# Performance work log

Measured on AMD Instinct MI355X. Metric: run time of the kernel, lower is better.

## Reference

```python
import jax, jax.numpy as jnp
import numpy as np

B, L, D, CH, H = 16384, 50, 20, 16, 6


def setup_inputs() -> dict:
    key = jax.random.key(0)
    ks = jax.random.split(key, 18)
    s = 0.1
    return {
        "x": jax.random.normal(ks[0], (B, L, D), jnp.float32),
        "we_w": jax.random.normal(ks[1], (CH, D), jnp.float32) * s,
        "we_b": jax.random.normal(ks[2], (CH,), jnp.float32) * s,
        "attn_w": jax.random.normal(ks[3], (CH, CH), jnp.float32) * s,
        "attn_b": jax.random.normal(ks[4], (CH,), jnp.float32) * s,
        "conv1_w": jax.random.normal(ks[5], (CH, CH, 1), jnp.float32) * s,
        "conv1_b": jax.random.normal(ks[6], (CH,), jnp.float32) * s,
        "conv2_w": jax.random.normal(ks[7], (CH, CH, 3), jnp.float32) * s,
        "conv2_b": jax.random.normal(ks[8], (CH,), jnp.float32) * s,
        "conv3_w": jax.random.normal(ks[9], (CH, CH, 5), jnp.float32) * s,
        "conv3_b": jax.random.normal(ks[10], (CH,), jnp.float32) * s,
        "gru_wih": jax.random.normal(ks[11], (3 * H, CH), jnp.float32) * s,
        "gru_whh": jax.random.normal(ks[12], (3 * H, H), jnp.float32) * s,
        "gru_bih": jax.random.normal(ks[13], (3 * H,), jnp.float32) * s,
        "gru_bhh": jax.random.normal(ks[14], (3 * H,), jnp.float32) * s,
        "fc3_w": jax.random.normal(ks[15], (2, 3 * CH + H), jnp.float32) * s,
        "fc3_b": jax.random.normal(ks[16], (2,), jnp.float32) * s,
        "batchsize": B,
    }


def _conv1d(x, w, b, pad):
    # x: [B, C, L], w: [O, I, K] -> [B, O, L]
    y = jax.lax.conv_general_dilated(x, w, (1,), [(pad, pad)],
                                     dimension_numbers=("NCH", "OIH", "NCH"))
    return y + b[None, :, None]


def _gru(xg, wih, whh, bih, bhh):
    # xg: [B, L, CH] -> outputs [B, L, H] (PyTorch GRU equations, h0=0)
    gi = jnp.einsum("blc,gc->blg", xg, wih) + bih  # [B, L, 3H]
    gi_t = jnp.swapaxes(gi, 0, 1)                  # [L, B, 3H]
    h0 = jnp.zeros((xg.shape[0], H), xg.dtype)

    def step(h, gi_step):
        gh = h @ whh.T + bhh
        i_r, i_z, i_n = jnp.split(gi_step, 3, axis=-1)
        h_r, h_z, h_n = jnp.split(gh, 3, axis=-1)
        r = jax.nn.sigmoid(i_r + h_r)
        z = jax.nn.sigmoid(i_z + h_z)
        n = jnp.tanh(i_n + r * h_n)
        h_new = (1.0 - z) * n + z * h
        return h_new, h_new

    _, outs = jax.lax.scan(step, h0, gi_t)
    return jnp.swapaxes(outs, 0, 1)  # [B, L, H]


def reference(x, we_w, we_b, attn_w, attn_b, conv1_w, conv1_b, conv2_w, conv2_b,
              conv3_w, conv3_b, gru_wih, gru_whh, gru_bih, gru_bhh, fc3_w, fc3_b,
              batchsize):
    b = batchsize
    xe = x @ we_w.T + we_b                 # [B, L, CH]
    xr = xe.reshape(b, CH, L)              # RESHAPE (not transpose), as in torch

    lrelu = lambda v: jnp.where(v > 0, v, 0.1 * v)
    x1 = lrelu(_conv1d(xr, conv1_w, conv1_b, 0))
    x2 = lrelu(_conv1d(xr, conv2_w, conv2_b, 1))
    x3 = lrelu(_conv1d(xr, conv3_w, conv3_b, 2))

    xg = xr.reshape(b, L, CH)              # == xe
    x4 = _gru(xg, gru_wih, gru_whh, gru_bih, gru_bhh)  # [B, L, H]

    # dotproduct1: note x4.reshape([B,H,L]) is a reshape, NOT a transpose
    scores = jnp.matmul(x4, x4.reshape(b, H, L)) / H   # [B, L, L]
    alphas = jax.nn.softmax(scores, axis=1)            # softmax over dim=1 as in torch
    y = jnp.matmul(alphas, x4).reshape(b, H, L)        # [B, H, L]
    x_gru = jnp.sum(y, axis=2)                         # [B, H]

    # vectorized per-timestep attention loop: x[:, :, i] over i -> swapaxes
    xt = jnp.swapaxes(xr, 1, 2)                        # [B, L, CH]
    attn = jnp.tanh(xt @ attn_w.T + attn_b)            # [B, L, CH]
    attn1 = jnp.concatenate([attn, attn, attn], axis=2).reshape(b, 3 * CH, L)

    x_cat = jnp.concatenate([x1, x2, x3], axis=1)      # [B, 3CH, L]
    x_cnn = jnp.sum(x_cat * attn1, axis=2)             # [B, 3CH]

    feat = jnp.concatenate([x_cnn, x_gru], axis=1)     # [B, 3CH+H]
    return feat @ fc3_w.T + fc3_b                      # [B, 2]
```

## Files before the change

### kernel.cpp

```cpp
#include <hip/hip_runtime.h>

#define BATCH 16384
#define LSEQ  50
#define DIN   20
#define CHN   16
#define HID   6

typedef float vf2 __attribute__((ext_vector_type(2)));

__device__ __forceinline__ float frcp(float x){ return __builtin_amdgcn_rcpf(x); }
__device__ __forceinline__ float fsig(float x){ return frcp(1.0f + __expf(-x)); }
__device__ __forceinline__ float ftanh(float x){ float t = __expf(2.0f*x); return (t - 1.0f) * frcp(t + 1.0f); }
__device__ __forceinline__ float lrelu(float v){ return v > 0.0f ? v : 0.1f*v; }
__device__ __forceinline__ vf2 fma2(vf2 a, vf2 b, vf2 c){
#if __has_builtin(__builtin_elementwise_fma)
  return __builtin_elementwise_fma(a, b, c);
#else
  vf2 r; r.x = fmaf(a.x, b.x, c.x); r.y = fmaf(a.y, b.y, c.y); return r;
#endif
}

constexpr int SLAB = 2544;

__global__ __launch_bounds__(256, 4) void fused_kernel(
    const float* __restrict__ x,
    const float* __restrict__ we_w, const float* __restrict__ we_b,
    const float* __restrict__ attn_w, const float* __restrict__ attn_b,
    const float* __restrict__ c1w, const float* __restrict__ c1b,
    const float* __restrict__ c2w, const float* __restrict__ c2b,
    const float* __restrict__ c3w, const float* __restrict__ c3b,
    const float* __restrict__ wih, const float* __restrict__ whh,
    const float* __restrict__ bih, const float* __restrict__ bhh,
    const float* __restrict__ fc3w, const float* __restrict__ fc3b,
    float* __restrict__ out)
{
  __shared__ __align__(16) float smem[4 * SLAB];
  const int tid  = threadIdx.x;
  const int wave = tid >> 6;
  const int lane = tid & 63;
  const int b    = blockIdx.x * 4 + wave;

  float* S    = smem + wave * SLAB;
  float* sXEp = S;
  float* sY   = S;
  float* R1   = S + 840;
  float* sFE  = S + 1640;
  float* sX4  = S + 1840;
  float* sX4P = S + 2144;

  const float* xb = x + (size_t)b * (LSEQ * DIN);

  if (lane < CHN) {
    sXEp[lane * 52]     = 0.0f;
    sXEp[lane * 52 + 1] = 0.0f;
  } else if (lane == 16) {
    sXEp[832] = 0.0f;
    sXEp[833] = 0.0f;
  }

  if (lane < LSEQ) {
    vf2 xv2[10];
    const float4* xr = (const float4*)(xb + lane * DIN);
    #pragma unroll
    for (int q = 0; q < 5; ++q) {
      float4 v = xr[q];
      vf2 p0; p0.x = v.x; p0.y = v.y;
      vf2 p1; p1.x = v.z; p1.y = v.w;
      xv2[2*q] = p0; xv2[2*q+1] = p1;
    }
    float xe[CHN];
    #pragma unroll
    for (int c = 0; c < CHN; ++c) {
      const vf2* wr = (const vf2*)(we_w + c * DIN);
      vf2 a2; a2.x = we_b[c]; a2.y = 0.0f;
      #pragma unroll
      for (int dp = 0; dp < 10; ++dp) a2 = fma2(xv2[dp], wr[dp], a2);
      xe[c] = a2.x + a2.y;
    }
    const int kk0 = lane * CHN;
    const int i0  = kk0 / 50;
    const int m0  = kk0 - i0 * 50;
    float* basep = sXEp + i0 * 52 + 2 + m0;
    #pragma unroll
    for (int c = 0; c < CHN; ++c) {
      const int off = c + ((m0 + c >= 50) ? 2 : 0);
      basep[off] = xe[c];
    }
    vf2 xe2[8];
    #pragma unroll
    for (int p = 0; p < 8; ++p) { xe2[p].x = xe[2*p]; xe2[p].y = xe[2*p+1]; }
    float gi[18];
    #pragma unroll
    for (int g = 0; g < 18; ++g) {
      const vf2* wr = (const vf2*)(wih + g * CHN);
      vf2 a2; a2.x = bih[g]; a2.y = 0.0f;
      #pragma unroll
      for (int p = 0; p < 8; ++p) a2 = fma2(xe2[p], wr[p], a2);
      gi[g] = a2.x + a2.y;
    }
    float4* gd = (float4*)(R1 + lane * 20);
    gd[0] = make_float4(gi[0], gi[1], gi[2], gi[3]);
    gd[1] = make_float4(gi[4], gi[5], gi[6], gi[7]);
    gd[2] = make_float4(gi[8], gi[9], gi[10], gi[11]);
    gd[3] = make_float4(gi[12], gi[13], gi[14], gi[15]);
    *(float2*)(R1 + lane * 20 + 16) = make_float2(gi[16], gi[17]);
  }
  __syncthreads();

  if (wave == 0) {
    const int q = lane >> 4;
    const int g = lane & 15;
    const int gb = 16 + (g & 1);
    float wa[HID], wb[HID];
    #pragma unroll
    for (int k = 0; k < HID; ++k) { wa[k] = whh[g * HID + k]; wb[k] = whh[gb * HID + k]; }
    const float ba = bhh[g];
    const float bb = bhh[gb];

    float* giq  = smem + q * SLAB + 840;
    float* x4q  = smem + q * SLAB + 1840;
    float* x4pq = smem + q * SLAB + 2144;

    const int base = q << 4;
    const int srcZ = base + 6 + g;
    const int srcN = base + ((g < 4) ? (12 + g) : (g - 4));

    float hh[HID];
    #pragma unroll
    for (int k = 0; k < HID; ++k) hh[k] = 0.0f;

    for (int l = 0; l < LSEQ; ++l) {
      const float gia = giq[l * 20 + g];
      const float gib = giq[l * 20 + gb];
      float gha = ba, ghb = bb;
      #pragma unroll
      for (int k = 0; k < HID; ++k) {
        gha = fmaf(wa[k], hh[k], gha);
        ghb = fmaf(wb[k], hh[k], ghb);
      }
      const float siga = fsig(gia + gha);
      const float ghx = (g >= 12) ? gha : ghb;
      const float gix = (g >= 12) ? gia : gib;
      const float ghn = __shfl(ghx, srcN);
      const float gin = __shfl(gix, srcN);
      const float z   = __shfl(siga, srcZ);
      const float n   = ftanh(fmaf(siga, ghn, gin));
      const float hn  = fmaf(z, hh[g < HID ? g : 0] - n, n);
      if (g < HID) {
        x4q[l * HID + g] = hn;
        x4pq[l * 8 + g]  = hn;
      }
      #pragma unroll
      for (int k = 0; k < HID; ++k) hh[k] = __shfl(hn, base + k);
    }
  }
  __syncthreads();

  if (lane < LSEQ) {
    float a[CHN];
    #pragma unroll
    for (int cc = 0; cc < CHN; ++cc) a[cc] = sXEp[cc * 52 + 2 + lane];
    vf2 a2[8];
    #pragma unroll
    for (int p = 0; p < 8; ++p) { a2[p].x = a[2*p]; a2[p].y = a[2*p+1]; }
    float o[CHN];
    #pragma unroll
    for (int c = 0; c < CHN; ++c) {
      const vf2* wr = (const vf2*)(attn_w + c * CHN);
      vf2 s2; s2.x = attn_b[c]; s2.y = 0.0f;
      #pragma unroll
      for (int p = 0; p < 8; ++p) s2 = fma2(a2[p], wr[p], s2);
      o[c] = ftanh(s2.x + s2.y);
    }
    float4* ad = (float4*)(R1 + lane * CHN);
    ad[0] = make_float4(o[0], o[1], o[2], o[3]);
    ad[1] = make_float4(o[4], o[5], o[6], o[7]);
    ad[2] = make_float4(o[8], o[9], o[10], o[11]);
    ad[3] = make_float4(o[12], o[13], o[14], o[15]);
  }
  __syncthreads();

  {
    float* sAT = R1;
    const int o   = lane & 15;
    const int seg = lane >> 4;
    const int s   = seg * 12;
    const int NL  = (seg == 3) ? 14 : 12;
    vf2 Z1[7], Z2[7], Z3[7];
    #pragma unroll
    for (int p = 0; p < 7; ++p) {
      Z1[p] = (vf2)0.0f; Z2[p] = (vf2)0.0f; Z3[p] = (vf2)0.0f;
    }
    for (int i = 0; i < CHN; ++i) {
      const float w1s = c1w[o * CHN + i];
      vf2 W1; W1.x = w1s; W1.y = w1s;
      vf2 W2[3], W3[5];
      #pragma unroll
      for (int t = 0; t < 3; ++t) { float w = c2w[(o * CHN + i) * 3 + t]; W2[t].x = w; W2[t].y = w; }
      #pragma unroll
      for (int t = 0; t < 5; ++t) { float w = c3w[(o * CHN + i) * 5 + t]; W3[t].x = w; W3[t].y = w; }
      const float4* wp = (const float4*)(sXEp + i * 52 + s);
      float4 q0 = wp[0], q1 = wp[1], q2 = wp[2], q3 = wp[3], q4 = wp[4];
      float xv[20] = {q0.x,q0.y,q0.z,q0.w, q1.x,q1.y,q1.z,q1.w,
                      q2.x,q2.y,q2.z,q2.w, q3.x,q3.y,q3.z,q3.w,
                      q4.x,q4.y,q4.z,q4.w};
      vf2 XP[17];
      #pragma unroll
      for (int a = 0; a < 17; ++a) { XP[a].x = xv[a]; XP[a].y = xv[a+1]; }
      #pragma unroll
      for (int p = 0; p < 7; ++p) {
        Z1[p] = fma2(W1, XP[2*p + 2], Z1[p]);
        Z2[p] = fma2(W2[0], XP[2*p + 1], Z2[p]);
        Z2[p] = fma2(W2[1], XP[2*p + 2], Z2[p]);
        Z2[p] = fma2(W2[2], XP[2*p + 3], Z2[p]);
        Z3[p] = fma2(W3[0], XP[2*p    ], Z3[p]);
        Z3[p] = fma2(W3[1], XP[2*p + 1], Z3[p]);
        Z3[p] = fma2(W3[2], XP[2*p + 2], Z3[p]);
        Z3[p] = fma2(W3[3], XP[2*p + 3], Z3[p]);
        Z3[p] = fma2(W3[4], XP[2*p + 4], Z3[p]);
      }
    }
    const float b1v = c1b[o], b2v = c2b[o], b3v = c3b[o];
    float a1 = 0.0f, a2 = 0.0f, a3 = 0.0f;
    #pragma unroll
    for (int u = 0; u < 14; ++u) {
      if (u < NL) {
        int l = s + u;
        float v1 = lrelu(Z1[u >> 1][u & 1] + b1v);
        float v2 = lrelu(Z2[u >> 1][u & 1] + b2v);
        float v3 = lrelu(Z3[u >> 1][u & 1] + b3v);
        int f1 = o * LSEQ + l;
        int f2 = (CHN + o) * LSEQ + l;
        int f3 = (2 * CHN + o) * LSEQ + l;
        a1 += v1 * sAT[(f1 / 48) * CHN + ((f1 % 48) & 15)];
        a2 += v2 * sAT[(f2 / 48) * CHN + ((f2 % 48) & 15)];
        a3 += v3 * sAT[(f3 / 48) * CHN + ((f3 % 48) & 15)];
      }
    }
    a1 += __shfl_xor(a1, 16); a1 += __shfl_xor(a1, 32);
    a2 += __shfl_xor(a2, 16); a2 += __shfl_xor(a2, 32);
    a3 += __shfl_xor(a3, 16); a3 += __shfl_xor(a3, 32);
    if (lane < CHN) { sFE[o] = a1; sFE[CHN + o] = a2; sFE[2 * CHN + o] = a3; }
  }
  __syncthreads();

  float* sC = R1;
  if (lane < LSEQ) {
    float colj[HID];
    #pragma unroll
    for (int h = 0; h < HID; ++h) colj[h] = sX4[h * LSEQ + lane];
    vf2 cj2[3];
    #pragma unroll
    for (int p = 0; p < 3; ++p) { cj2[p].x = colj[2*p]; cj2[p].y = colj[2*p+1]; }
    *(float4*)(sC + lane * 16)     = make_float4(colj[0], colj[1], colj[2], colj[3]);
    *(float2*)(sC + lane * 16 + 4) = make_float2(colj[4], colj[5]);
    float zs = 0.0f;
    for (int i = 0; i < LSEQ; ++i) {
      const float4 r0 = *(const float4*)(sX4P + i * 8);
      const float2 r1 = *(const float2*)(sX4P + i * 8 + 4);
      vf2 p0; p0.x = r0.x; p0.y = r0.y;
      vf2 p1; p1.x = r0.z; p1.y = r0.w;
      vf2 p2; p2.x = r1.x; p2.y = r1.y;
      vf2 s2 = (vf2)0.0f;
      s2 = fma2(p0, cj2[0], s2);
      s2 = fma2(p1, cj2[1], s2);
      s2 = fma2(p2, cj2[2], s2);
      zs += __expf((s2.x + s2.y) * (1.0f / 6.0f));
    }
    const float zi = frcp(zs);
    const float4 q0 = *(const float4*)(sX4P + lane * 8);
    const float2 q1 = *(const float2*)(sX4P + lane * 8 + 4);
    *(float4*)(sC + lane * 16 + 8)  = make_float4(zi*q0.x, zi*q0.y, zi*q0.z, zi*q0.w);
    *(float2*)(sC + lane * 16 + 12) = make_float2(zi*q1.x, zi*q1.y);
  }
  __syncthreads();

  if (lane < LSEQ) {
    vf2 ri2[3];
    {
      const float4 q0 = *(const float4*)(sX4P + lane * 8);
      const float2 q1 = *(const float2*)(sX4P + lane * 8 + 4);
      ri2[0].x = q0.x; ri2[0].y = q0.y;
      ri2[1].x = q0.z; ri2[1].y = q0.w;
      ri2[2].x = q1.x; ri2[2].y = q1.y;
    }
    vf2 ya2[3];
    #pragma unroll
    for (int p = 0; p < 3; ++p) ya2[p] = (vf2)0.0f;
    for (int j = 0; j < LSEQ; ++j) {
      const float4 t0 = *(const float4*)(sC + j * 16);
      const float2 t1 = *(const float2*)(sC + j * 16 + 4);
      vf2 p0; p0.x = t0.x; p0.y = t0.y;
      vf2 p1; p1.x = t0.z; p1.y = t0.w;
      vf2 p2; p2.x = t1.x; p2.y = t1.y;
      vf2 s2 = (vf2)0.0f;
      s2 = fma2(ri2[0], p0, s2);
      s2 = fma2(ri2[1], p1, s2);
      s2 = fma2(ri2[2], p2, s2);
      const float e = __expf((s2.x + s2.y) * (1.0f / 6.0f));
      vf2 e2; e2.x = e; e2.y = e;
      const float4 w0 = *(const float4*)(sC + j * 16 + 8);
      const float2 w1 = *(const float2*)(sC + j * 16 + 12);
      vf2 wv0; wv0.x = w0.x; wv0.y = w0.y;
      vf2 wv1; wv1.x = w0.z; wv1.y = w0.w;
      vf2 wv2; wv2.x = w1.x; wv2.y = w1.y;
      ya2[0] = fma2(e2, wv0, ya2[0]);
      ya2[1] = fma2(e2, wv1, ya2[1]);
      ya2[2] = fma2(e2, wv2, ya2[2]);
    }
    *(float2*)(sY + lane * 6)     = make_float2(ya2[0].x, ya2[0].y);
    *(float2*)(sY + lane * 6 + 2) = make_float2(ya2[1].x, ya2[1].y);
    *(float2*)(sY + lane * 6 + 4) = make_float2(ya2[2].x, ya2[2].y);
  }
  __syncthreads();

  if (lane < HID) {
    float s = 0.0f;
    for (int m = 0; m < LSEQ; ++m) s += sY[lane * LSEQ + m];
    sFE[48 + lane] = s;
  }
  __syncthreads();

  if (lane < 2) {
    float acc = fc3b[lane];
    const float* wr = fc3w + lane * 54;
    #pragma unroll
    for (int k = 0; k < 54; ++k) acc = fmaf(wr[k], sFE[k], acc);
    out[(size_t)b * 2 + lane] = acc;
  }
}

extern "C" void kernel_launch(void* const* d_in, const int* in_sizes, int n_in,
                              void* d_out, int out_size, void* d_ws, size_t ws_size,
                              hipStream_t stream) {
  (void)in_sizes; (void)n_in; (void)d_ws; (void)ws_size; (void)out_size;
  fused_kernel<<<BATCH / 4, 256, 0, stream>>>(
      (const float*)d_in[0],
      (const float*)d_in[1],  (const float*)d_in[2],
      (const float*)d_in[3],  (const float*)d_in[4],
      (const float*)d_in[5],  (const float*)d_in[6],
      (const float*)d_in[7],  (const float*)d_in[8],
      (const float*)d_in[9],  (const float*)d_in[10],
      (const float*)d_in[11], (const float*)d_in[12],
      (const float*)d_in[13], (const float*)d_in[14],
      (const float*)d_in[15], (const float*)d_in[16],
      (float*)d_out);
}
```

Baseline: 289.2 us.

## Run GRU per wave on its own sample and replace block barriers with wave fences

Previously wave 0 ran the GRU recurrence for all four samples in the block (16 lanes each), and the other waves idled at block-wide barriers. Now every wave runs the recurrence for its own sample in its own shared slab, so all block-wide __syncthreads can become wave-level barriers with compiler memory fences. This removes cross-wave barrier stalls and lets the four waves progress independently. The trade-off is that each wave now uses only 16 of its 64 lanes during the recurrence, and correctness relies on wave-local LDS ordering.

```diff
diff --git a/kernel.cpp b/kernel.cpp
--- a/kernel.cpp
+++ b/kernel.cpp
@@ -19,6 +19,7 @@
   vf2 r; r.x = fmaf(a.x, b.x, c.x); r.y = fmaf(a.y, b.y, c.y); return r;
 #endif
 }
+#define WFENCE() do { __builtin_amdgcn_wave_barrier(); __asm__ volatile("" ::: "memory"); } while (0)
 
 constexpr int SLAB = 2544;
 
@@ -105,10 +106,9 @@
     gd[3] = make_float4(gi[12], gi[13], gi[14], gi[15]);
     *(float2*)(R1 + lane * 20 + 16) = make_float2(gi[16], gi[17]);
   }
-  __syncthreads();
-
-  if (wave == 0) {
-    const int q = lane >> 4;
+  WFENCE();
+
+  {
     const int g = lane & 15;
     const int gb = 16 + (g & 1);
     float wa[HID], wb[HID];
@@ -117,21 +117,16 @@
     const float ba = bhh[g];
     const float bb = bhh[gb];
 
-    float* giq  = smem + q * SLAB + 840;
-    float* x4q  = smem + q * SLAB + 1840;
-    float* x4pq = smem + q * SLAB + 2144;
-
-    const int base = q << 4;
-    const int srcZ = base + 6 + g;
-    const int srcN = base + ((g < 4) ? (12 + g) : (g - 4));
+    const int srcZ = 6 + g;
+    const int srcN = (g < 4) ? (12 + g) : (g - 4);
 
     float hh[HID];
     #pragma unroll
     for (int k = 0; k < HID; ++k) hh[k] = 0.0f;
 
     for (int l = 0; l < LSEQ; ++l) {
-      const float gia = giq[l * 20 + g];
-      const float gib = giq[l * 20 + gb];
+      const float gia = R1[l * 20 + g];
+      const float gib = R1[l * 20 + gb];
       float gha = ba, ghb = bb;
       #pragma unroll
       for (int k = 0; k < HID; ++k) {
@@ -146,15 +141,15 @@
       const float z   = __shfl(siga, srcZ);
       const float n   = ftanh(fmaf(siga, ghn, gin));
       const float hn  = fmaf(z, hh[g < HID ? g : 0] - n, n);
-      if (g < HID) {
-        x4q[l * HID + g] = hn;
-        x4pq[l * 8 + g]  = hn;
+      if (lane < HID) {
+        sX4[l * HID + lane] = hn;
+        sX4P[l * 8 + lane]  = hn;
       }
       #pragma unroll
-      for (int k = 0; k < HID; ++k) hh[k] = __shfl(hn, base + k);
-    }
-  }
-  __syncthreads();
+      for (int k = 0; k < HID; ++k) hh[k] = __shfl(hn, k);
+    }
+  }
+  WFENCE();
 
   if (lane < LSEQ) {
     float a[CHN];
@@ -178,7 +173,7 @@
     ad[2] = make_float4(o[8], o[9], o[10], o[11]);
     ad[3] = make_float4(o[12], o[13], o[14], o[15]);
   }
-  __syncthreads();
+  WFENCE();
 
   {
     float* sAT = R1;
@@ -242,7 +237,7 @@
     a3 += __shfl_xor(a3, 16); a3 += __shfl_xor(a3, 32);
     if (lane < CHN) { sFE[o] = a1; sFE[CHN + o] = a2; sFE[2 * CHN + o] = a3; }
   }
-  __syncthreads();
+  WFENCE();
 
   float* sC = R1;
   if (lane < LSEQ) {
@@ -273,7 +268,7 @@
     *(float4*)(sC + lane * 16 + 8)  = make_float4(zi*q0.x, zi*q0.y, zi*q0.z, zi*q0.w);
     *(float2*)(sC + lane * 16 + 12) = make_float2(zi*q1.x, zi*q1.y);
   }
-  __syncthreads();
+  WFENCE();
 
   if (lane < LSEQ) {
     vf2 ri2[3];
@@ -312,14 +307,14 @@
     *(float2*)(sY + lane * 6 + 2) = make_float2(ya2[1].x, ya2[1].y);
     *(float2*)(sY + lane * 6 + 4) = make_float2(ya2[2].x, ya2[2].y);
   }
-  __syncthreads();
+  WFENCE();
 
   if (lane < HID) {
     float s = 0.0f;
     for (int m = 0; m < LSEQ; ++m) s += sY[lane * LSEQ + m];
     sFE[48 + lane] = s;
   }
-  __syncthreads();
+  WFENCE();
 
   if (lane < 2) {
     float acc = fc3b[lane];
```

Result: slower. 306.5 us (+6.0%).
